# Optimization experiments

Measured on AMD Instinct MI355X. Metric: run time of the kernel, lower is better.

The kernel has to match this reference:

```python
import jax, jax.numpy as jnp
import numpy as np

B, N, P, H, E, M, O, T = 4, 128, 512, 64, 32, 64, 64, 64

def _normalize(v, axis=-1, eps=1e-12):
    n = jnp.sqrt(jnp.sum(v * v, axis=axis, keepdims=True))
    return v / jnp.maximum(n, eps)

def _quat_mul(a, b):
    aw, ax, ay, az = a[..., 0], a[..., 1], a[..., 2], a[..., 3]
    bw, bx, by, bz = b[..., 0], b[..., 1], b[..., 2], b[..., 3]
    return jnp.stack([
        aw*bw - ax*bx - ay*by - az*bz,
        aw*bx + ax*bw + ay*bz - az*by,
        aw*by - ax*bz + ay*bw + az*bx,
        aw*bz + ax*by - ay*bx + az*bw], axis=-1)

def _quat_conj(q):
    return q * jnp.array([1.0, -1.0, -1.0, -1.0], dtype=q.dtype)

def _quat_rotate(q, v):
    # rotate vectors v [...,3] by unit quaternions q [...,4] in (w,x,y,z)
    qv = q[..., 1:]
    w = q[..., :1]
    t = 2.0 * jnp.cross(qv, v)
    return v + w * t + jnp.cross(qv, t)

def _mlp(x, W1, b1, W2, b2):
    return jax.nn.relu(x @ W1 + b1) @ W2 + b2

def setup_inputs():
    key = jax.random.key(0)
    ks = jax.random.split(key, 20)
    def w(k, i, o):
        return (jax.random.normal(k, (i, o), jnp.float32) / np.sqrt(i)).astype(jnp.float32)
    inp = dict(
        q=_normalize(jax.random.normal(ks[0], (B, N, 4), jnp.float32)),
        x=jax.random.normal(ks[1], (B, N, 3), jnp.float32),
        torsions=jax.random.normal(ks[2], (B, N, 7, 2), jnp.float32),
        h=jax.random.normal(ks[3], (B, N, H), jnp.float32),
        e=jax.random.normal(ks[4], (B, N, N, E), jnp.float32),
        node_mask=jnp.ones((B, N), bool),
        pocket_q=_normalize(jax.random.normal(ks[5], (B, P, 4), jnp.float32)),
        pocket_x=jax.random.normal(ks[6], (B, P, 3), jnp.float32),
        pocket_e=jax.random.normal(ks[7], (B, N, P, E), jnp.float32),
        pocket_h=jax.random.normal(ks[8], (B, P, H), jnp.float32),
        pocket_mask=jnp.ones((B, P), bool),
        Wm1=w(ks[9], 2 * H + E + 9, T), bm1=jnp.zeros((T,), jnp.float32),
        Wm2=w(ks[10], T, M), bm2=jnp.zeros((M,), jnp.float32),
        Wf1=w(ks[11], H + M, T), bf1=jnp.zeros((T,), jnp.float32),
        Wf2=w(ks[12], T, O), bf2=jnp.zeros((O,), jnp.float32),
        Wx1=w(ks[13], M, T), bx1=jnp.zeros((T,), jnp.float32),
        Wx2=w(ks[14], T, 3), bx2=jnp.zeros((3,), jnp.float32),
        Wq1=w(ks[15], M, T), bq1=jnp.zeros((T,), jnp.float32),
        Wq2=w(ks[16], T, 4), bq2=jnp.zeros((4,), jnp.float32),
        Wt1=w(ks[17], M, T), bt1=jnp.zeros((T,), jnp.float32),
        Wt2=w(ks[18], T, 14), bt2=jnp.zeros((14,), jnp.float32),
    )
    return inp

def _forward(q, x, torsions, h, e, pocket_q, pocket_x, pocket_e, pocket_h,
             node_mask, pocket_mask,
             Wm1, bm1, Wm2, bm2, Wf1, bf1, Wf2, bf2,
             Wx1, bx1, Wx2, bx2, Wq1, bq1, Wq2, bq2, Wt1, bt1, Wt2, bt2):
    b, n, hd = h.shape
    p = pocket_h.shape[-2]
    eye = jnp.eye(n, dtype=bool)
    pep_mm = node_mask[:, :, None] & node_mask[:, None, :] & (~eye)[None]
    poc_mm = node_mask[:, :, None] & pocket_mask[:, None, :]
    msg_mask = jnp.concatenate([pep_mm, poc_mm], axis=-1).astype(h.dtype)  # [B,N,N+P]
    n_neigh = (node_mask.sum(-1) + pocket_mask.sum(-1) - 1).astype(h.dtype)

    all_x = jnp.concatenate([x, pocket_x], axis=-2)   # [B,N+P,3]
    all_q = jnp.concatenate([q, pocket_q], axis=-2)   # [B,N+P,4]

    diff = x[:, :, None, :] - all_x[:, None, :, :]    # [B,N,N+P,3]
    d2 = jnp.sum(diff * diff, axis=-1)                # [B,N,N+P] == cat(peptide_d2, pocket_d2)
    qdot = jnp.abs(jnp.sum(q[:, :, None, :] * all_q[:, None, :, :], axis=-1))
    conj_j = _quat_conj(all_q)[:, None, :, :]         # inverse of frame j rotation
    local_x = _quat_rotate(conj_j, diff)              # R_j^T (x_i - x_j): global_to_local.apply
    local_q = _quat_mul(conj_j, q[:, :, None, :])     # q_j^{-1} * q_i

    hi = jnp.broadcast_to(h[:, :, None, :], (b, n, n + p, hd))
    hj = jnp.broadcast_to(jnp.concatenate([h, pocket_h], axis=-2)[:, None, :, :], (b, n, n + p, hd))
    e_all = jnp.concatenate([e, pocket_e], axis=-2)

    feat = jnp.concatenate([hi, hj, e_all, local_x, local_q, d2[..., None], qdot[..., None]], axis=-1)
    m = _mlp(feat, Wm1, bm1, Wm2, bm2) * msg_mask[..., None]
    msum = m.sum(axis=-2)                             # [B,N,M]

    o = _mlp(jnp.concatenate([h, msum], axis=-1), Wf1, bf1, Wf2, bf2)
    upd_torsions = _normalize(_mlp(msum, Wt1, bt1, Wt2, bt2).reshape(torsions.shape))

    dx = _mlp(m, Wx1, bx1, Wx2, bx2) * msg_mask[..., None]
    dq = _mlp(msum, Wq1, bq1, Wq2, bq2)
    ident = jnp.array([1.0, 0.0, 0.0, 0.0], dtype=dq.dtype)
    dq = jnp.where(node_mask[..., None], dq, ident)
    dq = _normalize(dq)
    upd_q = _quat_mul(q, dq)
    upd_q = jnp.where(node_mask[..., None], upd_q, ident)
    upd_q = _normalize(upd_q)                         # Rigid(Rotation(..., normalize_quats=True))

    rot_j = _normalize(all_q)[:, None, :, :]          # local->global rotation, normalize_quats=True
    upd_x = x + _quat_rotate(rot_j, dx).sum(axis=-2) / n_neigh[:, None, None]
    return upd_q, upd_x, upd_torsions, o

def reference(q, x, torsions, h, e, node_mask, pocket_q, pocket_x, pocket_e, pocket_h, pocket_mask,
              Wm1, bm1, Wm2, bm2, Wf1, bf1, Wf2, bf2,
              Wx1, bx1, Wx2, bx2, Wq1, bq1, Wq2, bq2, Wt1, bt1, Wt2, bt2):
    return _forward(q, x, torsions, h, e, pocket_q, pocket_x, pocket_e, pocket_h,
                    node_mask, pocket_mask,
                    Wm1, bm1, Wm2, bm2, Wf1, bf1, Wf2, bf2,
                    Wx1, bx1, Wx2, bx2, Wq1, bq1, Wq2, bq2, Wt1, bt1, Wt2, bt2)
```

## Files before the change

kernel.cpp:

```cpp
#include <hip/hip_runtime.h>
#include <stdint.h>

#define NB 4
#define NN 128
#define NP 512
#define NJ 640
#define HD 64
#define ED 32
#define NW 8

typedef unsigned short u16;
typedef __attribute__((ext_vector_type(8))) short short8;
typedef __attribute__((ext_vector_type(4))) float f32x4;

#define OFF_Q 0
#define OFF_X 2048
#define OFF_T 3584
#define OFF_O 10752

__device__ __forceinline__ uint32_t cvtpk(float a, float b) {
  uint32_t r;
  asm("v_cvt_pk_bf16_f32 %0, %1, %2" : "=v"(r) : "v"(a), "v"(b));
  return r;
}
__device__ __forceinline__ u16 bfh(float a) { return (u16)cvtpk(a, 0.f); }

__device__ __forceinline__ int w1row64(int k) {
  if (k < 32) return 128 + k;
  if (k < 35) return 160 + (k - 32);
  if (k < 39) return 163 + (k - 35);
  if (k == 39) return 167;
  if (k == 40) return 168;
  return -1;
}

__global__ void __launch_bounds__(256)
hj_pre(const float* __restrict__ h, const float* __restrict__ ph,
       const float* __restrict__ Wm1, float* __restrict__ HjW) {
  const int r = blockIdx.x * 4 + (threadIdx.x >> 6);
  const int lane = threadIdx.x & 63;
  const int b = r / NJ, j = r - b * NJ;
  const float* hr = (j < NN) ? h + ((size_t)(b * NN + j)) * HD
                             : ph + ((size_t)(b * NP + (j - NN))) * HD;
  float hv = hr[lane];
  float acc = 0.f;
#pragma unroll 16
  for (int k = 0; k < 64; ++k)
    acc += __shfl(hv, k) * Wm1[(size_t)(64 + k) * 64 + lane];
  HjW[((size_t)(b * 40 + (j >> 4))) * 1024 + lane * 16 + (j & 15)] = acc;
}

__global__ void __launch_bounds__(512, 2)
egnn_fused(const float* __restrict__ q, const float* __restrict__ x,
           const float* __restrict__ h, const float* __restrict__ e,
           const float* __restrict__ pe, const float* __restrict__ pq,
           const float* __restrict__ px, const float* __restrict__ ph,
           const float* __restrict__ HjW,
           const float* __restrict__ Wm1, const float* __restrict__ bm1,
           const float* __restrict__ Wm2, const float* __restrict__ bm2,
           const float* __restrict__ Wx1, const float* __restrict__ bx1,
           const float* __restrict__ Wx2, const float* __restrict__ bx2,
           const float* __restrict__ Wf1, const float* __restrict__ bf1,
           const float* __restrict__ Wf2, const float* __restrict__ bf2_,
           const float* __restrict__ Wq1, const float* __restrict__ bq1,
           const float* __restrict__ Wq2, const float* __restrict__ bq2,
           const float* __restrict__ Wt1, const float* __restrict__ bt1,
           const float* __restrict__ Wt2, const float* __restrict__ bt2,
           float* __restrict__ out)
{
  __shared__ __align__(16) u16 sW1B[64 * 64];
  __shared__ __align__(16) u16 sW2B[64 * 64];
  __shared__ __align__(16) u16 sWx1B[64 * 64];
  __shared__ __align__(16) u16 sB[NW][16 * 64];
  __shared__ float sRed[NW][64];
  __shared__ float sDx[NW][3];
  __shared__ float sHiP[64];

  const int b = blockIdx.x >> 7;
  const int i = blockIdx.x & 127;
  const int tid = threadIdx.x;
  const int wid = tid >> 6;
  const int lane = tid & 63;
  const int nl = lane & 15;
  const int quad = lane >> 4;
  const size_t node = (size_t)(b * NN + i);

  u16* sBw = sB[wid];
  float* sDxTw = sRed[wid];

  const int er = lane >> 2, ec = lane & 3;

  float4 EA, EB;
  {
    int jr = wid * 16 + er;
    const float* eb = (jr < NN)
        ? e + ((node * NN) + jr) * ED + ec * 8
        : pe + ((node * NP) + (jr - NN)) * ED + ec * 8;
    EA = *(const float4*)eb;
    EB = *(const float4*)(eb + 4);
  }

  for (int idx = tid; idx < 64 * 64; idx += 512) {
    int n = idx >> 6, k = idx & 63;
    int ks = k ^ ((n & 7) << 3);
    int row = w1row64(k);
    sW1B[n * 64 + ks]  = (row < 0) ? (u16)0 : bfh(Wm1[(size_t)row * 64 + n]);
    sW2B[n * 64 + ks]  = bfh(Wm2[(size_t)k * 64 + n]);
    sWx1B[n * 64 + ks] = bfh(Wx1[(size_t)k * 64 + n]);
  }
  for (int idx = lane; idx < 16 * 64 / 2; idx += 64) ((uint32_t*)sBw)[idx] = 0;

  if (tid >= 64 && tid < 128) {
    int col = tid - 64;
    float acc = bm1[col];
#pragma unroll 8
    for (int k = 0; k < HD; ++k) acc += h[node * HD + k] * Wm1[k * 64 + col];
    sHiP[col] = acc;
  }

  const float* qr0 = q + node * 4;
  const float qi0 = qr0[0], qi1 = qr0[1], qi2 = qr0[2], qi3 = qr0[3];
  const float* xr0 = x + node * 3;
  const float xi0 = xr0[0], xi1 = xr0[1], xi2 = xr0[2];

  short8 Wx2f[2];
#pragma unroll
  for (int ks = 0; ks < 2; ++ks) {
    const int k0 = ks * 32 + quad * 8;
    float v[8];
#pragma unroll
    for (int r = 0; r < 8; ++r) v[r] = (nl < 3) ? Wx2[(size_t)(k0 + r) * 3 + nl] : 0.f;
    union { uint32_t u[4]; short8 s; } cv;
    cv.u[0] = cvtpk(v[0], v[1]); cv.u[1] = cvtpk(v[2], v[3]);
    cv.u[2] = cvtpk(v[4], v[5]); cv.u[3] = cvtpk(v[6], v[7]);
    Wx2f[ks] = cv.s;
  }

  __syncthreads();

  float HiF[4], bm2F[4], bx1F[4];
#pragma unroll
  for (int nt = 0; nt < 4; ++nt) {
    HiF[nt] = sHiP[nt * 16 + nl];
    bm2F[nt] = bm2[nt * 16 + nl];
    bx1F[nt] = bx1[nt * 16 + nl];
  }
  const float bx2F = (nl < 3) ? bx2[nl] : 0.f;

  f32x4 msum[4];
#pragma unroll
  for (int nt = 0; nt < 4; ++nt) msum[nt] = (f32x4){0.f, 0.f, 0.f, 0.f};
  float dxs0 = 0.f, dxs1 = 0.f, dxs2 = 0.f;

  const int swr = (nl & 7) << 3;

  for (int tl = wid; tl < 40; tl += NW) {
    const int jb = tl * 16;

    const float* HjT = HjW + ((size_t)(b * 40 + tl)) * 1024;
    float4 hjv[4];
#pragma unroll
    for (int nt = 0; nt < 4; ++nt)
      hjv[nt] = *(const float4*)&HjT[(nt * 16 + nl) * 16 + quad * 4];

    float4 qj;
    float xj0 = 0.f, xj1 = 0.f, xj2 = 0.f;
    if (lane < 16) {
      int j = jb + lane;
      const float* qr = (j < NN) ? q + ((size_t)(b * NN + j)) * 4
                                 : pq + ((size_t)(b * NP + (j - NN))) * 4;
      qj = *(const float4*)qr;
      const float* xr = (j < NN) ? x + ((size_t)(b * NN + j)) * 3
                                 : px + ((size_t)(b * NP + (j - NN))) * 3;
      xj0 = xr[0]; xj1 = xr[1]; xj2 = xr[2];
    }

    {
      const int sw = (er & 7) << 3;
      uint4 pw;
      pw.x = cvtpk(EA.x, EA.y); pw.y = cvtpk(EA.z, EA.w);
      pw.z = cvtpk(EB.x, EB.y); pw.w = cvtpk(EB.z, EB.w);
      *(uint4*)&sBw[er * 64 + ((ec * 8) ^ sw)] = pw;
    }
    if (tl + NW < 40) {
      int jr2 = (tl + NW) * 16 + er;
      const float* eb = (jr2 < NN)
          ? e + ((node * NN) + jr2) * ED + ec * 8
          : pe + ((node * NP) + (jr2 - NN)) * ED + ec * 8;
      EA = *(const float4*)eb;
      EB = *(const float4*)(eb + 4);
    }

    float nqw = 0.f, nqx = 0.f, nqy = 0.f, nqz = 0.f;
    if (lane < 16) {
      float d0 = xi0 - xj0, d1 = xi1 - xj1, d2v = xi2 - xj2;
      float d2 = d0 * d0 + d1 * d1 + d2v * d2v;
      float qdot = fabsf(qi0 * qj.x + qi1 * qj.y + qi2 * qj.z + qi3 * qj.w);
      float ajw = qj.x, ajx = -qj.y, ajy = -qj.z, ajz = -qj.w;
      float t0 = 2.f * (ajy * d2v - ajz * d1);
      float t1 = 2.f * (ajz * d0 - ajx * d2v);
      float t2 = 2.f * (ajx * d1 - ajy * d0);
      float lx0 = d0 + ajw * t0 + (ajy * t2 - ajz * t1);
      float lx1 = d1 + ajw * t1 + (ajz * t0 - ajx * t2);
      float lx2 = d2v + ajw * t2 + (ajx * t1 - ajy * t0);
      float lqw = ajw * qi0 - ajx * qi1 - ajy * qi2 - ajz * qi3;
      float lqx = ajw * qi1 + ajx * qi0 + ajy * qi3 - ajz * qi2;
      float lqy = ajw * qi2 - ajx * qi3 + ajy * qi0 + ajz * qi1;
      float lqz = ajw * qi3 + ajx * qi2 - ajy * qi1 + ajz * qi0;
      float nn2 = qj.x * qj.x + qj.y * qj.y + qj.z * qj.z + qj.w * qj.w;
      float rn = 1.f / fmaxf(sqrtf(nn2), 1e-12f);
      nqw = qj.x * rn; nqx = qj.y * rn; nqy = qj.z * rn; nqz = qj.w * rn;
      uint4 g0, g1;
      g0.x = cvtpk(lx0, lx1); g0.y = cvtpk(lx2, lqw);
      g0.z = cvtpk(lqx, lqy); g0.w = cvtpk(lqz, d2);
      g1.x = cvtpk(qdot, 0.f); g1.y = 0; g1.z = 0; g1.w = 0;
      const int sw = (lane & 7) << 3;
      *(uint4*)&sBw[lane * 64 + (32 ^ sw)] = g0;
      *(uint4*)&sBw[lane * 64 + (40 ^ sw)] = g1;
    }

    f32x4 acc[4];
#pragma unroll
    for (int nt = 0; nt < 4; ++nt)
      acc[nt] = (f32x4){HiF[nt] + hjv[nt].x, HiF[nt] + hjv[nt].y,
                        HiF[nt] + hjv[nt].z, HiF[nt] + hjv[nt].w};
#pragma unroll
    for (int ks = 0; ks < 2; ++ks) {
      const int ko = (ks * 32 + quad * 8) ^ swr;
      short8 af = *(const short8*)&sBw[nl * 64 + ko];
#pragma unroll
      for (int nt = 0; nt < 4; ++nt) {
        short8 bfr = *(const short8*)&sW1B[(nt * 16 + nl) * 64 + ko];
        acc[nt] = __builtin_amdgcn_mfma_f32_16x16x32_bf16(af, bfr, acc[nt], 0, 0, 0);
      }
    }
#pragma unroll
    for (int r = 0; r < 4; ++r) {
      const int row = quad * 4 + r;
      const int sw2 = (row & 7) << 3;
#pragma unroll
      for (int nt = 0; nt < 4; ++nt)
        sBw[row * 64 + ((nt * 16 + nl) ^ sw2)] = bfh(fmaxf(acc[nt][r], 0.f));
    }

#pragma unroll
    for (int nt = 0; nt < 4; ++nt)
      acc[nt] = (f32x4){bm2F[nt], bm2F[nt], bm2F[nt], bm2F[nt]};
#pragma unroll
    for (int ks = 0; ks < 2; ++ks) {
      const int ko = (ks * 32 + quad * 8) ^ swr;
      short8 af = *(const short8*)&sBw[nl * 64 + ko];
#pragma unroll
      for (int nt = 0; nt < 4; ++nt) {
        short8 bfr = *(const short8*)&sW2B[(nt * 16 + nl) * 64 + ko];
        acc[nt] = __builtin_amdgcn_mfma_f32_16x16x32_bf16(af, bfr, acc[nt], 0, 0, 0);
      }
    }
#pragma unroll
    for (int r = 0; r < 4; ++r) {
      const int row = quad * 4 + r;
      const int sw2 = (row & 7) << 3;
#pragma unroll
      for (int nt = 0; nt < 4; ++nt) {
        float v = acc[nt][r];
        if (jb + row == i) v = 0.f;
        msum[nt][r] += v;
        sBw[row * 64 + ((nt * 16 + nl) ^ sw2)] = bfh(v);
      }
    }

#pragma unroll
    for (int nt = 0; nt < 4; ++nt)
      acc[nt] = (f32x4){bx1F[nt], bx1F[nt], bx1F[nt], bx1F[nt]};
#pragma unroll
    for (int ks = 0; ks < 2; ++ks) {
      const int ko = (ks * 32 + quad * 8) ^ swr;
      short8 af = *(const short8*)&sBw[nl * 64 + ko];
#pragma unroll
      for (int nt = 0; nt < 4; ++nt) {
        short8 bfr = *(const short8*)&sWx1B[(nt * 16 + nl) * 64 + ko];
        acc[nt] = __builtin_amdgcn_mfma_f32_16x16x32_bf16(af, bfr, acc[nt], 0, 0, 0);
      }
    }
#pragma unroll
    for (int r = 0; r < 4; ++r) {
      const int row = quad * 4 + r;
      const int sw2 = (row & 7) << 3;
#pragma unroll
      for (int nt = 0; nt < 4; ++nt)
        sBw[row * 64 + ((nt * 16 + nl) ^ sw2)] = bfh(fmaxf(acc[nt][r], 0.f));
    }

    f32x4 dacc = (f32x4){bx2F, bx2F, bx2F, bx2F};
#pragma unroll
    for (int ks = 0; ks < 2; ++ks) {
      const int ko = (ks * 32 + quad * 8) ^ swr;
      short8 af = *(const short8*)&sBw[nl * 64 + ko];
      dacc = __builtin_amdgcn_mfma_f32_16x16x32_bf16(af, Wx2f[ks], dacc, 0, 0, 0);
    }
    if (nl < 3) {
#pragma unroll
      for (int r = 0; r < 4; ++r) sDxTw[(quad * 4 + r) * 3 + nl] = dacc[r];
    }
    if (lane < 16) {
      int j = jb + lane;
      if (j != i) {
        float dxc0 = sDxTw[lane * 3 + 0];
        float dxc1 = sDxTw[lane * 3 + 1];
        float dxc2 = sDxTw[lane * 3 + 2];
        float rt0 = 2.f * (nqy * dxc2 - nqz * dxc1);
        float rt1 = 2.f * (nqz * dxc0 - nqx * dxc2);
        float rt2 = 2.f * (nqx * dxc1 - nqy * dxc0);
        dxs0 += dxc0 + nqw * rt0 + (nqy * rt2 - nqz * rt1);
        dxs1 += dxc1 + nqw * rt1 + (nqz * rt0 - nqx * rt2);
        dxs2 += dxc2 + nqw * rt2 + (nqx * rt1 - nqy * rt0);
      }
    }
  }

#pragma unroll
  for (int nt = 0; nt < 4; ++nt) {
    float s = msum[nt][0] + msum[nt][1] + msum[nt][2] + msum[nt][3];
    s += __shfl_xor(s, 16);
    s += __shfl_xor(s, 32);
    if (lane < 16) sRed[wid][nt * 16 + lane] = s;
  }
  {
    float a = dxs0, bb = dxs1, cc = dxs2;
#pragma unroll
    for (int off = 1; off < 16; off <<= 1) {
      a += __shfl_xor(a, off);
      bb += __shfl_xor(bb, off);
      cc += __shfl_xor(cc, off);
    }
    if (lane == 0) { sDx[wid][0] = a; sDx[wid][1] = bb; sDx[wid][2] = cc; }
  }
  __syncthreads();

  float* sPh3 = (float*)sB;
  if (wid == 0) {
    float ms = 0.f;
#pragma unroll
    for (int w = 0; w < NW; ++w) ms += sRed[w][lane];
    sPh3[0 * 64 + lane] = ms;
    float f1a = bf1[lane], f1b = 0.f;
    __syncwarp();
#pragma unroll 8
    for (int k = 0; k < 64; ++k) {
      f1a += h[node * HD + k] * Wf1[k * 64 + lane];
      f1b += sPh3[0 * 64 + k] * Wf1[(64 + k) * 64 + lane];
    }
    float f1 = fmaxf(f1a + f1b, 0.f);
    __syncwarp();
    sPh3[0 * 64 + lane] = f1;
    float oacc = bf2_[lane];
    __syncwarp();
#pragma unroll 8
    for (int k = 0; k < 64; ++k) oacc += sPh3[0 * 64 + k] * Wf2[k * 64 + lane];
    out[OFF_O + node * 64 + lane] = oacc;
  } else if (wid == 1) {
    float ms = 0.f;
#pragma unroll
    for (int w = 0; w < NW; ++w) ms += sRed[w][lane];
    sPh3[1 * 64 + lane] = ms;
    float a = bq1[lane];
    __syncwarp();
#pragma unroll 8
    for (int k = 0; k < 64; ++k) a += sPh3[1 * 64 + k] * Wq1[k * 64 + lane];
    a = fmaxf(a, 0.f);
    float p0 = a * Wq2[lane * 4 + 0];
    float p1 = a * Wq2[lane * 4 + 1];
    float p2 = a * Wq2[lane * 4 + 2];
    float p3 = a * Wq2[lane * 4 + 3];
#pragma unroll
    for (int off = 32; off >= 1; off >>= 1) {
      p0 += __shfl_xor(p0, off);
      p1 += __shfl_xor(p1, off);
      p2 += __shfl_xor(p2, off);
      p3 += __shfl_xor(p3, off);
    }
    float dq0 = p0 + bq2[0], dq1 = p1 + bq2[1];
    float dq2 = p2 + bq2[2], dq3 = p3 + bq2[3];
    float n = fmaxf(sqrtf(dq0 * dq0 + dq1 * dq1 + dq2 * dq2 + dq3 * dq3), 1e-12f);
    dq0 /= n; dq1 /= n; dq2 /= n; dq3 /= n;
    float uw = qi0 * dq0 - qi1 * dq1 - qi2 * dq2 - qi3 * dq3;
    float ux = qi0 * dq1 + qi1 * dq0 + qi2 * dq3 - qi3 * dq2;
    float uy = qi0 * dq2 - qi1 * dq3 + qi2 * dq0 + qi3 * dq1;
    float uz = qi0 * dq3 + qi1 * dq2 - qi2 * dq1 + qi3 * dq0;
    float n2 = fmaxf(sqrtf(uw * uw + ux * ux + uy * uy + uz * uz), 1e-12f);
    if (lane == 0) {
      float* po = out + OFF_Q + node * 4;
      po[0] = uw / n2; po[1] = ux / n2; po[2] = uy / n2; po[3] = uz / n2;
    }
  } else if (wid == 2) {
    float ms = 0.f;
#pragma unroll
    for (int w = 0; w < NW; ++w) ms += sRed[w][lane];
    sPh3[2 * 64 + lane] = ms;
    float a = bt1[lane];
    __syncwarp();
#pragma unroll 8
    for (int k = 0; k < 64; ++k) a += sPh3[2 * 64 + k] * Wt1[k * 64 + lane];
    a = fmaxf(a, 0.f);
    __syncwarp();
    sPh3[2 * 64 + lane] = a;
    __syncwarp();
    if (lane < 14) {
      float v = bt2[lane];
#pragma unroll 8
      for (int k = 0; k < 64; ++k) v += sPh3[2 * 64 + k] * Wt2[k * 14 + lane];
      float pv = __shfl_xor(v, 1);
      float nrm = fmaxf(sqrtf(v * v + pv * pv), 1e-12f);
      out[OFF_T + node * 14 + lane] = v / nrm;
    }
  } else if (wid == 3) {
    if (lane < 3) {
      float xs = 0.f;
#pragma unroll
      for (int w = 0; w < NW; ++w) xs += sDx[w][lane];
      float xiv = (lane == 0) ? xi0 : (lane == 1) ? xi1 : xi2;
      out[OFF_X + node * 3 + lane] = xiv + xs / 639.0f;
    }
  }
}

extern "C" void kernel_launch(void* const* d_in, const int* in_sizes, int n_in,
                              void* d_out, int out_size, void* d_ws, size_t ws_size,
                              hipStream_t stream) {
  const float* q   = (const float*)d_in[0];
  const float* x   = (const float*)d_in[1];
  const float* h   = (const float*)d_in[3];
  const float* e   = (const float*)d_in[4];
  const float* pq  = (const float*)d_in[6];
  const float* px  = (const float*)d_in[7];
  const float* pe  = (const float*)d_in[8];
  const float* ph  = (const float*)d_in[9];
  const float* Wm1 = (const float*)d_in[11];
  const float* bm1 = (const float*)d_in[12];
  const float* Wm2 = (const float*)d_in[13];
  const float* bm2 = (const float*)d_in[14];
  const float* Wf1 = (const float*)d_in[15];
  const float* bf1 = (const float*)d_in[16];
  const float* Wf2 = (const float*)d_in[17];
  const float* bf2_ = (const float*)d_in[18];
  const float* Wx1 = (const float*)d_in[19];
  const float* bx1 = (const float*)d_in[20];
  const float* Wx2 = (const float*)d_in[21];
  const float* bx2 = (const float*)d_in[22];
  const float* Wq1 = (const float*)d_in[23];
  const float* bq1 = (const float*)d_in[24];
  const float* Wq2 = (const float*)d_in[25];
  const float* bq2 = (const float*)d_in[26];
  const float* Wt1 = (const float*)d_in[27];
  const float* bt1 = (const float*)d_in[28];
  const float* Wt2 = (const float*)d_in[29];
  const float* bt2 = (const float*)d_in[30];

  float* HjW = (float*)d_ws;

  hj_pre<<<NB * NJ / 4, 256, 0, stream>>>(h, ph, Wm1, HjW);
  egnn_fused<<<NB * NN, 512, 0, stream>>>(
      q, x, h, e, pe, pq, px, ph, HjW,
      Wm1, bm1, Wm2, bm2, Wx1, bx1, Wx2, bx2,
      Wf1, bf1, Wf2, bf2_, Wq1, bq1, Wq2, bq2,
      Wt1, bt1, Wt2, bt2, (float*)d_out);
}
```

Baseline: 191.1 us.

## Interleave two independent tiles per warp to overlap MFMA chains

```diff
diff --git a/kernel.cpp b/kernel.cpp
--- a/kernel.cpp
+++ b/kernel.cpp
@@ -50,7 +50,7 @@
   HjW[((size_t)(b * 40 + (j >> 4))) * 1024 + lane * 16 + (j & 15)] = acc;
 }
 
-__global__ void __launch_bounds__(512, 2)
+__global__ void __launch_bounds__(512, 1)
 egnn_fused(const float* __restrict__ q, const float* __restrict__ x,
            const float* __restrict__ h, const float* __restrict__ e,
            const float* __restrict__ pe, const float* __restrict__ pq,
@@ -71,7 +71,9 @@
   __shared__ __align__(16) u16 sW1B[64 * 64];
   __shared__ __align__(16) u16 sW2B[64 * 64];
   __shared__ __align__(16) u16 sWx1B[64 * 64];
-  __shared__ __align__(16) u16 sB[NW][16 * 64];
+  __shared__ __align__(16) u16 sBA[NW][16 * 64];
+  __shared__ __align__(16) u16 sBB[NW][16 * 64];
+  __shared__ float sDxT[NW][2][16][3];
   __shared__ float sRed[NW][64];
   __shared__ float sDx[NW][3];
   __shared__ float sHiP[64];
@@ -85,20 +87,31 @@
   const int quad = lane >> 4;
   const size_t node = (size_t)(b * NN + i);
 
-  u16* sBw = sB[wid];
-  float* sDxTw = sRed[wid];
+  u16* sB0w = sBA[wid];
+  u16* sB1w = sBB[wid];
 
   const int er = lane >> 2, ec = lane & 3;
-
-  float4 EA, EB;
-  {
-    int jr = wid * 16 + er;
+  const int swr = (nl & 7) << 3;
+
+  auto eload = [&](float4& A, float4& Bv, int jb) {
+    int jr = jb + er;
     const float* eb = (jr < NN)
         ? e + ((node * NN) + jr) * ED + ec * 8
         : pe + ((node * NP) + (jr - NN)) * ED + ec * 8;
-    EA = *(const float4*)eb;
-    EB = *(const float4*)(eb + 4);
-  }
+    A = *(const float4*)eb;
+    Bv = *(const float4*)(eb + 4);
+  };
+  auto packE = [&](u16* sBx, const float4& A, const float4& Bv) {
+    const int sw = (er & 7) << 3;
+    uint4 pw;
+    pw.x = cvtpk(A.x, A.y); pw.y = cvtpk(A.z, A.w);
+    pw.z = cvtpk(Bv.x, Bv.y); pw.w = cvtpk(Bv.z, Bv.w);
+    *(uint4*)&sBx[er * 64 + ((ec * 8) ^ sw)] = pw;
+  };
+
+  float4 E0A, E0B, E1A, E1B;
+  eload(E0A, E0B, wid * 16);
+  eload(E1A, E1B, (wid + 8) * 16);
 
   for (int idx = tid; idx < 64 * 64; idx += 512) {
     int n = idx >> 6, k = idx & 63;
@@ -108,7 +121,10 @@
     sW2B[n * 64 + ks]  = bfh(Wm2[(size_t)k * 64 + n]);
     sWx1B[n * 64 + ks] = bfh(Wx1[(size_t)k * 64 + n]);
   }
-  for (int idx = lane; idx < 16 * 64 / 2; idx += 64) ((uint32_t*)sBw)[idx] = 0;
+  for (int idx = lane; idx < 512; idx += 64) {
+    ((uint32_t*)sB0w)[idx] = 0;
+    ((uint32_t*)sB1w)[idx] = 0;
+  }
 
   if (tid >= 64 && tid < 128) {
     int col = tid - 64;
@@ -152,47 +168,16 @@
   for (int nt = 0; nt < 4; ++nt) msum[nt] = (f32x4){0.f, 0.f, 0.f, 0.f};
   float dxs0 = 0.f, dxs1 = 0.f, dxs2 = 0.f;
 
-  const int swr = (nl & 7) << 3;
-
-  for (int tl = wid; tl < 40; tl += NW) {
-    const int jb = tl * 16;
-
-    const float* HjT = HjW + ((size_t)(b * 40 + tl)) * 1024;
-    float4 hjv[4];
-#pragma unroll
-    for (int nt = 0; nt < 4; ++nt)
-      hjv[nt] = *(const float4*)&HjT[(nt * 16 + nl) * 16 + quad * 4];
-
-    float4 qj;
-    float xj0 = 0.f, xj1 = 0.f, xj2 = 0.f;
+  auto geo = [&](u16* sBx, int jb, float& nqw, float& nqx, float& nqy, float& nqz) {
+    nqw = nqx = nqy = nqz = 0.f;
     if (lane < 16) {
       int j = jb + lane;
       const float* qr = (j < NN) ? q + ((size_t)(b * NN + j)) * 4
                                  : pq + ((size_t)(b * NP + (j - NN))) * 4;
-      qj = *(const float4*)qr;
+      float4 qj = *(const float4*)qr;
       const float* xr = (j < NN) ? x + ((size_t)(b * NN + j)) * 3
                                  : px + ((size_t)(b * NP + (j - NN))) * 3;
-      xj0 = xr[0]; xj1 = xr[1]; xj2 = xr[2];
-    }
-
-    {
-      const int sw = (er & 7) << 3;
-      uint4 pw;
-      pw.x = cvtpk(EA.x, EA.y); pw.y = cvtpk(EA.z, EA.w);
-      pw.z = cvtpk(EB.x, EB.y); pw.w = cvtpk(EB.z, EB.w);
-      *(uint4*)&sBw[er * 64 + ((ec * 8) ^ sw)] = pw;
-    }
-    if (tl + NW < 40) {
-      int jr2 = (tl + NW) * 16 + er;
-      const float* eb = (jr2 < NN)
-          ? e + ((node * NN) + jr2) * ED + ec * 8
-          : pe + ((node * NP) + (jr2 - NN)) * ED + ec * 8;
-      EA = *(const float4*)eb;
-      EB = *(const float4*)(eb + 4);
-    }
-
-    float nqw = 0.f, nqx = 0.f, nqy = 0.f, nqz = 0.f;
-    if (lane < 16) {
+      float xj0 = xr[0], xj1 = xr[1], xj2 = xr[2];
       float d0 = xi0 - xj0, d1 = xi1 - xj1, d2v = xi2 - xj2;
       float d2 = d0 * d0 + d1 * d1 + d2v * d2v;
       float qdot = fabsf(qi0 * qj.x + qi1 * qj.y + qi2 * qj.z + qi3 * qj.w);
@@ -215,47 +200,33 @@
       g0.z = cvtpk(lqx, lqy); g0.w = cvtpk(lqz, d2);
       g1.x = cvtpk(qdot, 0.f); g1.y = 0; g1.z = 0; g1.w = 0;
       const int sw = (lane & 7) << 3;
-      *(uint4*)&sBw[lane * 64 + (32 ^ sw)] = g0;
-      *(uint4*)&sBw[lane * 64 + (40 ^ sw)] = g1;
-    }
-
-    f32x4 acc[4];
-#pragma unroll
-    for (int nt = 0; nt < 4; ++nt)
-      acc[nt] = (f32x4){HiF[nt] + hjv[nt].x, HiF[nt] + hjv[nt].y,
-                        HiF[nt] + hjv[nt].z, HiF[nt] + hjv[nt].w};
+      *(uint4*)&sBx[lane * 64 + (32 ^ sw)] = g0;
+      *(uint4*)&sBx[lane * 64 + (40 ^ sw)] = g1;
+    }
+  };
+  auto mfmaPhase = [&](const u16* sBx, const u16* W, f32x4* acc) {
 #pragma unroll
     for (int ks = 0; ks < 2; ++ks) {
       const int ko = (ks * 32 + quad * 8) ^ swr;
-      short8 af = *(const short8*)&sBw[nl * 64 + ko];
+      short8 af = *(const short8*)&sBx[nl * 64 + ko];
 #pragma unroll
       for (int nt = 0; nt < 4; ++nt) {
-        short8 bfr = *(const short8*)&sW1B[(nt * 16 + nl) * 64 + ko];
+        short8 bfr = *(const short8*)&W[(nt * 16 + nl) * 64 + ko];
         acc[nt] = __builtin_amdgcn_mfma_f32_16x16x32_bf16(af, bfr, acc[nt], 0, 0, 0);
       }
     }
+  };
+  auto storeRelu = [&](u16* sBx, const f32x4* acc) {
 #pragma unroll
     for (int r = 0; r < 4; ++r) {
       const int row = quad * 4 + r;
       const int sw2 = (row & 7) << 3;
 #pragma unroll
       for (int nt = 0; nt < 4; ++nt)
-        sBw[row * 64 + ((nt * 16 + nl) ^ sw2)] = bfh(fmaxf(acc[nt][r], 0.f));
-    }
-
-#pragma unroll
-    for (int nt = 0; nt < 4; ++nt)
-      acc[nt] = (f32x4){bm2F[nt], bm2F[nt], bm2F[nt], bm2F[nt]};
-#pragma unroll
-    for (int ks = 0; ks < 2; ++ks) {
-      const int ko = (ks * 32 + quad * 8) ^ swr;
-      short8 af = *(const short8*)&sBw[nl * 64 + ko];
-#pragma unroll
-      for (int nt = 0; nt < 4; ++nt) {
-        short8 bfr = *(const short8*)&sW2B[(nt * 16 + nl) * 64 + ko];
-        acc[nt] = __builtin_amdgcn_mfma_f32_16x16x32_bf16(af, bfr, acc[nt], 0, 0, 0);
-      }
-    }
+        sBx[row * 64 + ((nt * 16 + nl) ^ sw2)] = bfh(fmaxf(acc[nt][r], 0.f));
+    }
+  };
+  auto storeL2 = [&](u16* sBx, const f32x4* acc, int jb) {
 #pragma unroll
     for (int r = 0; r < 4; ++r) {
       const int row = quad * 4 + r;
@@ -265,49 +236,30 @@
         float v = acc[nt][r];
         if (jb + row == i) v = 0.f;
         msum[nt][r] += v;
-        sBw[row * 64 + ((nt * 16 + nl) ^ sw2)] = bfh(v);
+        sBx[row * 64 + ((nt * 16 + nl) ^ sw2)] = bfh(v);
       }
     }
-
-#pragma unroll
-    for (int nt = 0; nt < 4; ++nt)
-      acc[nt] = (f32x4){bx1F[nt], bx1F[nt], bx1F[nt], bx1F[nt]};
+  };
+  auto x2Phase = [&](const u16* sBx, f32x4& dacc) {
 #pragma unroll
     for (int ks = 0; ks < 2; ++ks) {
       const int ko = (ks * 32 + quad * 8) ^ swr;
-      short8 af = *(const short8*)&sBw[nl * 64 + ko];
-#pragma unroll
-      for (int nt = 0; nt < 4; ++nt) {
-        short8 bfr = *(const short8*)&sWx1B[(nt * 16 + nl) * 64 + ko];
-        acc[nt] = __builtin_amdgcn_mfma_f32_16x16x32_bf16(af, bfr, acc[nt], 0, 0, 0);
-      }
-    }
-#pragma unroll
-    for (int r = 0; r < 4; ++r) {
-      const int row = quad * 4 + r;
-      const int sw2 = (row & 7) << 3;
-#pragma unroll
-      for (int nt = 0; nt < 4; ++nt)
-        sBw[row * 64 + ((nt * 16 + nl) ^ sw2)] = bfh(fmaxf(acc[nt][r], 0.f));
-    }
-
-    f32x4 dacc = (f32x4){bx2F, bx2F, bx2F, bx2F};
-#pragma unroll
-    for (int ks = 0; ks < 2; ++ks) {
-      const int ko = (ks * 32 + quad * 8) ^ swr;
-      short8 af = *(const short8*)&sBw[nl * 64 + ko];
+      short8 af = *(const short8*)&sBx[nl * 64 + ko];
       dacc = __builtin_amdgcn_mfma_f32_16x16x32_bf16(af, Wx2f[ks], dacc, 0, 0, 0);
     }
+  };
+  auto dxFinish = [&](int reg, int jb, const f32x4& dacc,
+                      float nqw, float nqx, float nqy, float nqz) {
     if (nl < 3) {
 #pragma unroll
-      for (int r = 0; r < 4; ++r) sDxTw[(quad * 4 + r) * 3 + nl] = dacc[r];
+      for (int r = 0; r < 4; ++r) sDxT[wid][reg][quad * 4 + r][nl] = dacc[r];
     }
     if (lane < 16) {
       int j = jb + lane;
       if (j != i) {
-        float dxc0 = sDxTw[lane * 3 + 0];
-        float dxc1 = sDxTw[lane * 3 + 1];
-        float dxc2 = sDxTw[lane * 3 + 2];
+        float dxc0 = sDxT[wid][reg][lane][0];
+        float dxc1 = sDxT[wid][reg][lane][1];
+        float dxc2 = sDxT[wid][reg][lane][2];
         float rt0 = 2.f * (nqy * dxc2 - nqz * dxc1);
         float rt1 = 2.f * (nqz * dxc0 - nqx * dxc2);
         float rt2 = 2.f * (nqx * dxc1 - nqy * dxc0);
@@ -316,6 +268,104 @@
         dxs2 += dxc2 + nqw * rt2 + (nqx * rt1 - nqy * rt0);
       }
     }
+  };
+  auto hjGather = [&](int tl, float4* hjv) {
+    const float* HjT = HjW + ((size_t)(b * 40 + tl)) * 1024;
+#pragma unroll
+    for (int nt = 0; nt < 4; ++nt)
+      hjv[nt] = *(const float4*)&HjT[(nt * 16 + nl) * 16 + quad * 4];
+  };
+
+#pragma unroll 1
+  for (int p = 0; p < 2; ++p) {
+    const int ta = wid + p * 16, tb = ta + 8;
+    const int jba = ta * 16, jbb = tb * 16;
+
+    float4 hja[4], hjb[4];
+    hjGather(ta, hja);
+    hjGather(tb, hjb);
+
+    packE(sB0w, E0A, E0B);
+    packE(sB1w, E1A, E1B);
+    if (p == 0) {
+      eload(E0A, E0B, (wid + 16) * 16);
+      eload(E1A, E1B, (wid + 24) * 16);
+    } else {
+      eload(E0A, E0B, (wid + 32) * 16);
+    }
+
+    float nqwa, nqxa, nqya, nqza, nqwb, nqxb, nqyb, nqzb;
+    geo(sB0w, jba, nqwa, nqxa, nqya, nqza);
+    geo(sB1w, jbb, nqwb, nqxb, nqyb, nqzb);
+
+    f32x4 accA[4], accB[4];
+#pragma unroll
+    for (int nt = 0; nt < 4; ++nt) {
+      accA[nt] = (f32x4){HiF[nt] + hja[nt].x, HiF[nt] + hja[nt].y,
+                         HiF[nt] + hja[nt].z, HiF[nt] + hja[nt].w};
+      accB[nt] = (f32x4){HiF[nt] + hjb[nt].x, HiF[nt] + hjb[nt].y,
+                         HiF[nt] + hjb[nt].z, HiF[nt] + hjb[nt].w};
+    }
+    mfmaPhase(sB0w, sW1B, accA);
+    mfmaPhase(sB1w, sW1B, accB);
+    storeRelu(sB0w, accA);
+    storeRelu(sB1w, accB);
+
+#pragma unroll
+    for (int nt = 0; nt < 4; ++nt) {
+      accA[nt] = (f32x4){bm2F[nt], bm2F[nt], bm2F[nt], bm2F[nt]};
+      accB[nt] = (f32x4){bm2F[nt], bm2F[nt], bm2F[nt], bm2F[nt]};
+    }
+    mfmaPhase(sB0w, sW2B, accA);
+    mfmaPhase(sB1w, sW2B, accB);
+    storeL2(sB0w, accA, jba);
+    storeL2(sB1w, accB, jbb);
+
+#pragma unroll
+    for (int nt = 0; nt < 4; ++nt) {
+      accA[nt] = (f32x4){bx1F[nt], bx1F[nt], bx1F[nt], bx1F[nt]};
+      accB[nt] = (f32x4){bx1F[nt], bx1F[nt], bx1F[nt], bx1F[nt]};
+    }
+    mfmaPhase(sB0w, sWx1B, accA);
+    mfmaPhase(sB1w, sWx1B, accB);
+    storeRelu(sB0w, accA);
+    storeRelu(sB1w, accB);
+
+    f32x4 dA = (f32x4){bx2F, bx2F, bx2F, bx2F};
+    f32x4 dB = (f32x4){bx2F, bx2F, bx2F, bx2F};
+    x2Phase(sB0w, dA);
+    x2Phase(sB1w, dB);
+    dxFinish(0, jba, dA, nqwa, nqxa, nqya, nqza);
+    dxFinish(1, jbb, dB, nqwb, nqxb, nqyb, nqzb);
+  }
+
+  {
+    const int tl = wid + 32, jb = tl * 16;
+    float4 hj[4];
+    hjGather(tl, hj);
+    packE(sB0w, E0A, E0B);
+    float nqw, nqx, nqy, nqz;
+    geo(sB0w, jb, nqw, nqx, nqy, nqz);
+    f32x4 acc[4];
+#pragma unroll
+    for (int nt = 0; nt < 4; ++nt)
+      acc[nt] = (f32x4){HiF[nt] + hj[nt].x, HiF[nt] + hj[nt].y,
+                        HiF[nt] + hj[nt].z, HiF[nt] + hj[nt].w};
+    mfmaPhase(sB0w, sW1B, acc);
+    storeRelu(sB0w, acc);
+#pragma unroll
+    for (int nt = 0; nt < 4; ++nt)
+      acc[nt] = (f32x4){bm2F[nt], bm2F[nt], bm2F[nt], bm2F[nt]};
+    mfmaPhase(sB0w, sW2B, acc);
+    storeL2(sB0w, acc, jb);
+#pragma unroll
+    for (int nt = 0; nt < 4; ++nt)
+      acc[nt] = (f32x4){bx1F[nt], bx1F[nt], bx1F[nt], bx1F[nt]};
+    mfmaPhase(sB0w, sWx1B, acc);
+    storeRelu(sB0w, acc);
+    f32x4 d = (f32x4){bx2F, bx2F, bx2F, bx2F};
+    x2Phase(sB0w, d);
+    dxFinish(0, jb, d, nqw, nqx, nqy, nqz);
   }
 
 #pragma unroll
@@ -337,7 +387,7 @@
   }
   __syncthreads();
 
-  float* sPh3 = (float*)sB;
+  float* sPh3 = (float*)sBA;
   if (wid == 0) {
     float ms = 0.f;
 #pragma unroll
```

New measurement: 197.2 us. +3.2%, slower.

## Split fused EGNN kernel into two half-node blocks plus separate epilogue kernel

Applied to the files above, without the earlier changes.

```diff
diff --git a/kernel.cpp b/kernel.cpp
--- a/kernel.cpp
+++ b/kernel.cpp
@@ -7,7 +7,6 @@
 #define NJ 640
 #define HD 64
 #define ED 32
-#define NW 8
 
 typedef unsigned short u16;
 typedef __attribute__((ext_vector_type(8))) short short8;
@@ -17,6 +16,9 @@
 #define OFF_X 2048
 #define OFF_T 3584
 #define OFF_O 10752
+
+#define HJ_FLOATS (NB * 40 * 1024)
+#define P_STRIDE 68
 
 __device__ __forceinline__ uint32_t cvtpk(float a, float b) {
   uint32_t r;
@@ -50,66 +52,59 @@
   HjW[((size_t)(b * 40 + (j >> 4))) * 1024 + lane * 16 + (j & 15)] = acc;
 }
 
-__global__ void __launch_bounds__(512, 2)
-egnn_fused(const float* __restrict__ q, const float* __restrict__ x,
-           const float* __restrict__ h, const float* __restrict__ e,
-           const float* __restrict__ pe, const float* __restrict__ pq,
-           const float* __restrict__ px, const float* __restrict__ ph,
-           const float* __restrict__ HjW,
-           const float* __restrict__ Wm1, const float* __restrict__ bm1,
-           const float* __restrict__ Wm2, const float* __restrict__ bm2,
-           const float* __restrict__ Wx1, const float* __restrict__ bx1,
-           const float* __restrict__ Wx2, const float* __restrict__ bx2,
-           const float* __restrict__ Wf1, const float* __restrict__ bf1,
-           const float* __restrict__ Wf2, const float* __restrict__ bf2_,
-           const float* __restrict__ Wq1, const float* __restrict__ bq1,
-           const float* __restrict__ Wq2, const float* __restrict__ bq2,
-           const float* __restrict__ Wt1, const float* __restrict__ bt1,
-           const float* __restrict__ Wt2, const float* __restrict__ bt2,
-           float* __restrict__ out)
+__global__ void __launch_bounds__(256, 4)
+egnn_main(const float* __restrict__ q, const float* __restrict__ x,
+          const float* __restrict__ h, const float* __restrict__ e,
+          const float* __restrict__ pe, const float* __restrict__ pq,
+          const float* __restrict__ px, const float* __restrict__ ph,
+          const float* __restrict__ HjW,
+          const float* __restrict__ Wm1, const float* __restrict__ bm1,
+          const float* __restrict__ Wm2, const float* __restrict__ bm2,
+          const float* __restrict__ Wx1, const float* __restrict__ bx1,
+          const float* __restrict__ Wx2, const float* __restrict__ bx2,
+          float* __restrict__ Pp)
 {
   __shared__ __align__(16) u16 sW1B[64 * 64];
   __shared__ __align__(16) u16 sW2B[64 * 64];
   __shared__ __align__(16) u16 sWx1B[64 * 64];
-  __shared__ __align__(16) u16 sB[NW][16 * 64];
-  __shared__ float sRed[NW][64];
-  __shared__ float sDx[NW][3];
-  __shared__ float sHiP[64];
-
-  const int b = blockIdx.x >> 7;
-  const int i = blockIdx.x & 127;
+  __shared__ __align__(16) u16 sB[4][16 * 64];
+
+  const int bid = blockIdx.x;
+  const int half = bid & 1;
+  const int nid = bid >> 1;
+  const int b = nid >> 7;
+  const int i = nid & 127;
   const int tid = threadIdx.x;
   const int wid = tid >> 6;
   const int lane = tid & 63;
   const int nl = lane & 15;
   const int quad = lane >> 4;
-  const size_t node = (size_t)(b * NN + i);
+  const size_t node = (size_t)nid;
 
   u16* sBw = sB[wid];
-  float* sDxTw = sRed[wid];
-
+  const int slot = half * 4 + wid;
   const int er = lane >> 2, ec = lane & 3;
+  const int swr = (nl & 7) << 3;
 
   float4 EA, EB;
   {
-    int jr = wid * 16 + er;
-    const float* eb = (jr < NN)
+    int jr = slot * 16 + er;
+    const float* ebp = (jr < NN)
         ? e + ((node * NN) + jr) * ED + ec * 8
         : pe + ((node * NP) + (jr - NN)) * ED + ec * 8;
-    EA = *(const float4*)eb;
-    EB = *(const float4*)(eb + 4);
-  }
-
-  for (int idx = tid; idx < 64 * 64; idx += 512) {
-    int n = idx >> 6, k = idx & 63;
-    int ks = k ^ ((n & 7) << 3);
-    int row = w1row64(k);
+    EA = *(const float4*)ebp;
+    EB = *(const float4*)(ebp + 4);
+  }
+
+  for (int idx = tid; idx < 64 * 64; idx += 256) {
+    int n = idx >> 6, k2 = idx & 63;
+    int ks = k2 ^ ((n & 7) << 3);
+    int row = w1row64(k2);
     sW1B[n * 64 + ks]  = (row < 0) ? (u16)0 : bfh(Wm1[(size_t)row * 64 + n]);
-    sW2B[n * 64 + ks]  = bfh(Wm2[(size_t)k * 64 + n]);
-    sWx1B[n * 64 + ks] = bfh(Wx1[(size_t)k * 64 + n]);
-  }
-  for (int idx = lane; idx < 16 * 64 / 2; idx += 64) ((uint32_t*)sBw)[idx] = 0;
-
+    sW2B[n * 64 + ks]  = bfh(Wm2[(size_t)k2 * 64 + n]);
+    sWx1B[n * 64 + ks] = bfh(Wx1[(size_t)k2 * 64 + n]);
+  }
+  float* sHiP = (float*)sB;
   if (tid >= 64 && tid < 128) {
     int col = tid - 64;
     float acc = bm1[col];
@@ -147,14 +142,18 @@
   }
   const float bx2F = (nl < 3) ? bx2[nl] : 0.f;
 
+  __syncthreads();
+  for (int idx = lane; idx < 512; idx += 64) ((uint32_t*)sBw)[idx] = 0;
+
   f32x4 msum[4];
 #pragma unroll
   for (int nt = 0; nt < 4; ++nt) msum[nt] = (f32x4){0.f, 0.f, 0.f, 0.f};
   float dxs0 = 0.f, dxs1 = 0.f, dxs2 = 0.f;
 
-  const int swr = (nl & 7) << 3;
-
-  for (int tl = wid; tl < 40; tl += NW) {
+  float* sDxTw = (float*)sBw;
+
+  for (int kk = 0; kk < 5; ++kk) {
+    const int tl = slot + kk * 8;
     const int jb = tl * 16;
 
     const float* HjT = HjW + ((size_t)(b * 40 + tl)) * 1024;
@@ -182,13 +181,13 @@
       pw.z = cvtpk(EB.x, EB.y); pw.w = cvtpk(EB.z, EB.w);
       *(uint4*)&sBw[er * 64 + ((ec * 8) ^ sw)] = pw;
     }
-    if (tl + NW < 40) {
-      int jr2 = (tl + NW) * 16 + er;
-      const float* eb = (jr2 < NN)
+    if (kk < 4) {
+      int jr2 = (slot + (kk + 1) * 8) * 16 + er;
+      const float* ebp = (jr2 < NN)
           ? e + ((node * NN) + jr2) * ED + ec * 8
           : pe + ((node * NP) + (jr2 - NN)) * ED + ec * 8;
-      EA = *(const float4*)eb;
-      EB = *(const float4*)(eb + 4);
+      EA = *(const float4*)ebp;
+      EB = *(const float4*)(ebp + 4);
     }
 
     float nqw = 0.f, nqx = 0.f, nqy = 0.f, nqz = 0.f;
@@ -318,12 +317,13 @@
     }
   }
 
+  float* sMy = (float*)sBw;
 #pragma unroll
   for (int nt = 0; nt < 4; ++nt) {
     float s = msum[nt][0] + msum[nt][1] + msum[nt][2] + msum[nt][3];
     s += __shfl_xor(s, 16);
     s += __shfl_xor(s, 32);
-    if (lane < 16) sRed[wid][nt * 16 + lane] = s;
+    if (lane < 16) sMy[nt * 16 + lane] = s;
   }
   {
     float a = dxs0, bb = dxs1, cc = dxs2;
@@ -333,40 +333,69 @@
       bb += __shfl_xor(bb, off);
       cc += __shfl_xor(cc, off);
     }
-    if (lane == 0) { sDx[wid][0] = a; sDx[wid][1] = bb; sDx[wid][2] = cc; }
+    if (lane == 0) { sMy[64] = a; sMy[65] = bb; sMy[66] = cc; }
   }
   __syncthreads();
 
-  float* sPh3 = (float*)sB;
+  float* sAll = (float*)sB;
   if (wid == 0) {
-    float ms = 0.f;
-#pragma unroll
-    for (int w = 0; w < NW; ++w) ms += sRed[w][lane];
-    sPh3[0 * 64 + lane] = ms;
+    float t = sAll[0 * 512 + lane] + sAll[1 * 512 + lane] +
+              sAll[2 * 512 + lane] + sAll[3 * 512 + lane];
+    Pp[(size_t)bid * P_STRIDE + lane] = t;
+  } else if (wid == 1) {
+    if (lane < 3) {
+      float t = sAll[0 * 512 + 64 + lane] + sAll[1 * 512 + 64 + lane] +
+                sAll[2 * 512 + 64 + lane] + sAll[3 * 512 + 64 + lane];
+      Pp[(size_t)bid * P_STRIDE + 64 + lane] = t;
+    }
+  }
+}
+
+__global__ void __launch_bounds__(256, 1)
+egnn_epi(const float* __restrict__ q, const float* __restrict__ x,
+         const float* __restrict__ h, const float* __restrict__ Pp,
+         const float* __restrict__ Wf1, const float* __restrict__ bf1,
+         const float* __restrict__ Wf2, const float* __restrict__ bf2_,
+         const float* __restrict__ Wq1, const float* __restrict__ bq1,
+         const float* __restrict__ Wq2, const float* __restrict__ bq2,
+         const float* __restrict__ Wt1, const float* __restrict__ bt1,
+         const float* __restrict__ Wt2, const float* __restrict__ bt2,
+         float* __restrict__ out)
+{
+  __shared__ float sE[3][64];
+  const int n = blockIdx.x;
+  const int tid = threadIdx.x;
+  const int wid = tid >> 6;
+  const int lane = tid & 63;
+  const size_t node = (size_t)n;
+  const float* P0 = Pp + (size_t)(n * 2) * P_STRIDE;
+  const float* P1 = P0 + P_STRIDE;
+
+  if (wid == 0) {
+    float ms = P0[lane] + P1[lane];
+    sE[0][lane] = ms;
     float f1a = bf1[lane], f1b = 0.f;
     __syncwarp();
 #pragma unroll 8
     for (int k = 0; k < 64; ++k) {
       f1a += h[node * HD + k] * Wf1[k * 64 + lane];
-      f1b += sPh3[0 * 64 + k] * Wf1[(64 + k) * 64 + lane];
+      f1b += sE[0][k] * Wf1[(64 + k) * 64 + lane];
     }
     float f1 = fmaxf(f1a + f1b, 0.f);
     __syncwarp();
-    sPh3[0 * 64 + lane] = f1;
+    sE[0][lane] = f1;
     float oacc = bf2_[lane];
     __syncwarp();
 #pragma unroll 8
-    for (int k = 0; k < 64; ++k) oacc += sPh3[0 * 64 + k] * Wf2[k * 64 + lane];
+    for (int k = 0; k < 64; ++k) oacc += sE[0][k] * Wf2[k * 64 + lane];
     out[OFF_O + node * 64 + lane] = oacc;
   } else if (wid == 1) {
-    float ms = 0.f;
-#pragma unroll
-    for (int w = 0; w < NW; ++w) ms += sRed[w][lane];
-    sPh3[1 * 64 + lane] = ms;
+    float ms = P0[lane] + P1[lane];
+    sE[1][lane] = ms;
     float a = bq1[lane];
     __syncwarp();
 #pragma unroll 8
-    for (int k = 0; k < 64; ++k) a += sPh3[1 * 64 + k] * Wq1[k * 64 + lane];
+    for (int k = 0; k < 64; ++k) a += sE[1][k] * Wq1[k * 64 + lane];
     a = fmaxf(a, 0.f);
     float p0 = a * Wq2[lane * 4 + 0];
     float p1 = a * Wq2[lane * 4 + 1];
@@ -381,8 +410,10 @@
     }
     float dq0 = p0 + bq2[0], dq1 = p1 + bq2[1];
     float dq2 = p2 + bq2[2], dq3 = p3 + bq2[3];
-    float n = fmaxf(sqrtf(dq0 * dq0 + dq1 * dq1 + dq2 * dq2 + dq3 * dq3), 1e-12f);
-    dq0 /= n; dq1 /= n; dq2 /= n; dq3 /= n;
+    float nn = fmaxf(sqrtf(dq0 * dq0 + dq1 * dq1 + dq2 * dq2 + dq3 * dq3), 1e-12f);
+    dq0 /= nn; dq1 /= nn; dq2 /= nn; dq3 /= nn;
+    const float qi0 = q[node * 4 + 0], qi1 = q[node * 4 + 1];
+    const float qi2 = q[node * 4 + 2], qi3 = q[node * 4 + 3];
     float uw = qi0 * dq0 - qi1 * dq1 - qi2 * dq2 - qi3 * dq3;
     float ux = qi0 * dq1 + qi1 * dq0 + qi2 * dq3 - qi3 * dq2;
     float uy = qi0 * dq2 - qi1 * dq3 + qi2 * dq0 + qi3 * dq1;
@@ -393,33 +424,28 @@
       po[0] = uw / n2; po[1] = ux / n2; po[2] = uy / n2; po[3] = uz / n2;
     }
   } else if (wid == 2) {
-    float ms = 0.f;
-#pragma unroll
-    for (int w = 0; w < NW; ++w) ms += sRed[w][lane];
-    sPh3[2 * 64 + lane] = ms;
+    float ms = P0[lane] + P1[lane];
+    sE[2][lane] = ms;
     float a = bt1[lane];
     __syncwarp();
 #pragma unroll 8
-    for (int k = 0; k < 64; ++k) a += sPh3[2 * 64 + k] * Wt1[k * 64 + lane];
+    for (int k = 0; k < 64; ++k) a += sE[2][k] * Wt1[k * 64 + lane];
     a = fmaxf(a, 0.f);
     __syncwarp();
-    sPh3[2 * 64 + lane] = a;
+    sE[2][lane] = a;
     __syncwarp();
     if (lane < 14) {
       float v = bt2[lane];
 #pragma unroll 8
-      for (int k = 0; k < 64; ++k) v += sPh3[2 * 64 + k] * Wt2[k * 14 + lane];
+      for (int k = 0; k < 64; ++k) v += sE[2][k] * Wt2[k * 14 + lane];
       float pv = __shfl_xor(v, 1);
       float nrm = fmaxf(sqrtf(v * v + pv * pv), 1e-12f);
       out[OFF_T + node * 14 + lane] = v / nrm;
     }
-  } else if (wid == 3) {
+  } else {
     if (lane < 3) {
-      float xs = 0.f;
-#pragma unroll
-      for (int w = 0; w < NW; ++w) xs += sDx[w][lane];
-      float xiv = (lane == 0) ? xi0 : (lane == 1) ? xi1 : xi2;
-      out[OFF_X + node * 3 + lane] = xiv + xs / 639.0f;
+      float xs = P0[64 + lane] + P1[64 + lane];
+      out[OFF_X + node * 3 + lane] = x[node * 3 + lane] + xs / 639.0f;
     }
   }
 }
@@ -457,11 +483,13 @@
   const float* bt2 = (const float*)d_in[30];
 
   float* HjW = (float*)d_ws;
+  float* Pp  = HjW + HJ_FLOATS;
 
   hj_pre<<<NB * NJ / 4, 256, 0, stream>>>(h, ph, Wm1, HjW);
-  egnn_fused<<<NB * NN, 512, 0, stream>>>(
+  egnn_main<<<NB * NN * 2, 256, 0, stream>>>(
       q, x, h, e, pe, pq, px, ph, HjW,
-      Wm1, bm1, Wm2, bm2, Wx1, bx1, Wx2, bx2,
-      Wf1, bf1, Wf2, bf2_, Wq1, bq1, Wq2, bq2,
+      Wm1, bm1, Wm2, bm2, Wx1, bx1, Wx2, bx2, Pp);
+  egnn_epi<<<NB * NN, 256, 0, stream>>>(
+      q, x, h, Pp, Wf1, bf1, Wf2, bf2_, Wq1, bq1, Wq2, bq2,
       Wt1, bt1, Wt2, bt2, (float*)d_out);
 }
```

New measurement: 242.0 us. 1.27x slower.
